# Performance work log

Hardware: AMD Instinct MI355X
Metric: run time of the kernel (lower is better)

## Reference

```python
import jax, jax.numpy as jnp
import numpy as np

N = 100000
E = 1600000
F_IN = 128
HDIM = 64
HEADS = 8
C1 = HDIM // HEADS  # 8 per-head channels in conv1
NUM_CLASSES = 2
NUM_GRAPHS = 64
NEG_SLOPE = 0.2


def setup_inputs() -> dict:
    key = jax.random.key(0)
    ks = jax.random.split(key, 12)
    x = jax.random.normal(ks[0], (N, F_IN), dtype=jnp.float32)
    edge_index = jax.random.randint(ks[1], (2, E), 0, N, dtype=jnp.int64)
    batch = jnp.sort(jax.random.randint(ks[2], (N,), 0, NUM_GRAPHS, dtype=jnp.int64))
    # conv1 params (Glorot-ish scale)
    W1 = jax.random.normal(ks[3], (F_IN, HEADS * C1), dtype=jnp.float32) * (1.0 / np.sqrt(F_IN))
    att_src1 = jax.random.normal(ks[4], (HEADS, C1), dtype=jnp.float32) * 0.1
    att_dst1 = jax.random.normal(ks[5], (HEADS, C1), dtype=jnp.float32) * 0.1
    b1 = jnp.zeros((HEADS * C1,), dtype=jnp.float32)
    # conv2 params (1 head, no concat)
    W2 = jax.random.normal(ks[6], (HDIM, 1 * NUM_CLASSES), dtype=jnp.float32) * (1.0 / np.sqrt(HDIM))
    att_src2 = jax.random.normal(ks[7], (1, NUM_CLASSES), dtype=jnp.float32) * 0.1
    att_dst2 = jax.random.normal(ks[8], (1, NUM_CLASSES), dtype=jnp.float32) * 0.1
    b2 = jnp.zeros((NUM_CLASSES,), dtype=jnp.float32)
    return {"x": x, "edge_index": edge_index, "batch": batch,
            "W1": W1, "att_src1": att_src1, "att_dst1": att_dst1, "b1": b1,
            "W2": W2, "att_src2": att_src2, "att_dst2": att_dst2, "b2": b2}


def gat_conv(x, src, dst, W, a_src, a_dst, b, heads, ch, concat):
    # PyG GATConv: linear proj -> per-edge attention -> segment softmax over dst -> scatter-add
    n = x.shape[0]
    h = (x @ W).reshape(n, heads, ch)                      # [N,H,C]
    alpha_s = jnp.einsum('nhc,hc->nh', h, a_src)           # [N,H]
    alpha_d = jnp.einsum('nhc,hc->nh', h, a_dst)           # [N,H]
    e = jax.nn.leaky_relu(alpha_s[src] + alpha_d[dst], NEG_SLOPE)  # [E,H]
    m = jax.ops.segment_max(e, dst, num_segments=n)        # stable softmax per dst
    e = jnp.exp(e - m[dst])
    denom = jax.ops.segment_sum(e, dst, num_segments=n) + 1e-16
    alpha = e / denom[dst]                                 # [E,H]
    msg = h[src] * alpha[:, :, None]                       # [E,H,C]
    out = jax.ops.segment_sum(msg, dst, num_segments=n)    # [N,H,C]
    if concat:
        out = out.reshape(n, heads * ch)
    else:
        out = out.mean(axis=1)
    return out + b


def reference(x, edge_index, batch, W1, att_src1, att_dst1, b1, W2, att_src2, att_dst2, b2):
    # PyG GATConv default add_self_loops=True
    loops = jnp.arange(N, dtype=edge_index.dtype)
    src = jnp.concatenate([edge_index[0], loops])
    dst = jnp.concatenate([edge_index[1], loops])
    h = gat_conv(x, src, dst, W1, att_src1, att_dst1, b1, HEADS, C1, concat=True)
    h = jax.nn.relu(h)
    # F.dropout with training=False (eval mode) -> identity
    h = gat_conv(h, src, dst, W2, att_src2, att_dst2, b2, 1, NUM_CLASSES, concat=False)
    # global_mean_pool over batch ids
    sums = jax.ops.segment_sum(h, batch, num_segments=NUM_GRAPHS)
    cnts = jax.ops.segment_sum(jnp.ones((N,), h.dtype), batch, num_segments=NUM_GRAPHS)
    pooled = sums / jnp.maximum(cnts, 1.0)[:, None]        # [G, num_classes]
    return jax.nn.log_softmax(pooled, axis=1)
```

## Files before the change

### kernel.cpp

```cpp
#include <hip/hip_runtime.h>
#include <hip/hip_bf16.h>
#include <hip/hip_fp16.h>
#include <math.h>

#define NN 100000
#define EE 1600000
#define ET 1700000
#define NEG_SLOPE 0.2f
#define XS_STRIDE 136

#define BKB 8
#define BKSZ 256
#define NBUCK 391
#define SLAB 8192
#define PAD 32
#define EPT2 16
#define CHUNK2 (256 * EPT2)
#define NCH2 ((ET + CHUNK2 - 1) / CHUNK2)

typedef _Float16 f16;
typedef f16 f16x8 __attribute__((ext_vector_type(8)));
typedef float f32x4 __attribute__((ext_vector_type(4)));

__device__ __forceinline__ float leaky(float v) {
    return v > 0.f ? v : NEG_SLOPE * v;
}
__device__ __forceinline__ unsigned char enc_fp8(float v) {
    int pk = __builtin_amdgcn_cvt_pk_fp8_f32(v, 0.f, 0, false);
    return (unsigned char)(pk & 0xff);
}

__global__ __launch_bounds__(256) void convert_w_kernel(
        const float* __restrict__ W1, f16* __restrict__ wt) {
    int i = blockIdx.x * 256 + threadIdx.x;
    if (i < 128 * 64) {
        int n = i >> 7, k = i & 127;
        wt[n * 128 + k] = (f16)W1[k * 64 + n];
    }
}

__global__ __launch_bounds__(256) void gemm1_mfma(
        const float* __restrict__ x, const f16* __restrict__ wt,
        const float* __restrict__ att_s, const float* __restrict__ att_d,
        unsigned char* __restrict__ h1f8, __half* __restrict__ as1h,
        float* __restrict__ ad1o) {
    __shared__ f16 xs[64 * XS_STRIDE];
    const int tid = threadIdx.x;
    const int node0 = blockIdx.x * 64;
    for (int i = tid; i < 64 * 64; i += 256) {
        int r = i >> 6, cp = i & 63;
        int n = node0 + r;
        float2 v = (n < NN) ? ((const float2*)x)[(long)n * 64 + cp]
                            : make_float2(0.f, 0.f);
        xs[r * XS_STRIDE + 2 * cp]     = (f16)v.x;
        xs[r * XS_STRIDE + 2 * cp + 1] = (f16)v.y;
    }
    __syncthreads();
    const int wv = tid >> 6;
    const int lane = tid & 63;
    const int n16 = lane & 15;
    const int quad = lane >> 4;
    f16x8 bf[4][4];
#pragma unroll
    for (int t = 0; t < 4; ++t)
#pragma unroll
        for (int kk = 0; kk < 4; ++kk)
            bf[t][kk] = *(const f16x8*)(wt + ((t * 16 + n16) * 128 + kk * 32 + quad * 8));
    f32x4 acc[4] = {{0,0,0,0},{0,0,0,0},{0,0,0,0},{0,0,0,0}};
#pragma unroll
    for (int kk = 0; kk < 4; ++kk) {
        f16x8 af = *(const f16x8*)(xs + ((wv * 16 + n16) * XS_STRIDE + kk * 32 + quad * 8));
#pragma unroll
        for (int t = 0; t < 4; ++t)
            acc[t] = __builtin_amdgcn_mfma_f32_16x16x32_f16(af, bf[t][kk], acc[t], 0, 0, 0);
    }
    float ats[4], atd[4];
#pragma unroll
    for (int t = 0; t < 4; ++t) {
        ats[t] = att_s[t * 16 + n16];
        atd[t] = att_d[t * 16 + n16];
    }
#pragma unroll
    for (int t = 0; t < 4; ++t)
#pragma unroll
        for (int r = 0; r < 4; ++r) {
            int m = node0 + wv * 16 + quad * 4 + r;
            bool ok = (m < NN);
            if (ok) h1f8[m * 64 + t * 16 + n16] = enc_fp8(acc[t][r]);
            float vs = acc[t][r] * ats[t];
            float vd = acc[t][r] * atd[t];
            vs += __shfl_xor(vs, 1, 64); vd += __shfl_xor(vd, 1, 64);
            vs += __shfl_xor(vs, 2, 64); vd += __shfl_xor(vd, 2, 64);
            vs += __shfl_xor(vs, 4, 64); vd += __shfl_xor(vd, 4, 64);
            if (ok && (n16 & 7) == 0) {
                int h = t * 2 + (n16 >> 3);
                as1h[m * 8 + h] = __float2half_rn(vs);
                ad1o[m * 8 + h] = vd;
            }
        }
}

__global__ __launch_bounds__(256) void bucket_fill(
        const int* __restrict__ ei, int* __restrict__ bcur,
        unsigned* __restrict__ gpay) {
    __shared__ int lcnt[NBUCK];
    __shared__ int gbase[NBUCK];
    const int tid = threadIdx.x;
    for (int i = tid; i < NBUCK; i += 256) lcnt[i] = 0;
    __syncthreads();
    const int base = blockIdx.x * CHUNK2 + tid;
    unsigned pay[EPT2];
    int bk[EPT2], pos[EPT2];
#pragma unroll
    for (int k = 0; k < EPT2; ++k) {
        int e = base + k * 256;
        if (e < ET) {
            int s, d;
            if (e < EE) {
                s = __builtin_nontemporal_load(ei + e);
                d = __builtin_nontemporal_load(ei + EE + e);
            } else { s = d = e - EE; }
            int b = d >> BKB;
            bk[k] = b;
            pay[k] = ((unsigned)(d & (BKSZ - 1)) << 17) | (unsigned)s;
            pos[k] = atomicAdd(&lcnt[b], 1);
        } else bk[k] = -1;
    }
    __syncthreads();
    for (int i = tid; i < NBUCK; i += 256)
        gbase[i] = lcnt[i] ? (i * SLAB + atomicAdd(&bcur[i * PAD], lcnt[i])) : 0;
    __syncthreads();
#pragma unroll
    for (int k = 0; k < EPT2; ++k)
        if (bk[k] >= 0) gpay[gbase[bk[k]] + pos[k]] = pay[k];
}

__global__ __launch_bounds__(256) void fine_csr(
        const unsigned* __restrict__ gpay, const int* __restrict__ bcur,
        int* __restrict__ rowptr, int* __restrict__ rowend,
        int* __restrict__ csr_src) {
    __shared__ int cnt[BKSZ];
    __shared__ int ts[256];
    const int b = blockIdx.x;
    const int tid = threadIdx.x;
    const int off = b * SLAB;
    int blen = bcur[b * PAD];
    if (blen > SLAB) blen = SLAB;
    const int d0 = b << BKB;
    cnt[tid] = 0;
    __syncthreads();
    for (int i = tid; i < blen; i += 256)
        atomicAdd(&cnt[gpay[off + i] >> 17], 1);
    __syncthreads();
    int v = cnt[tid];
    ts[tid] = v;
    __syncthreads();
    for (int o = 1; o < 256; o <<= 1) {
        int u = (tid >= o) ? ts[tid - o] : 0;
        __syncthreads();
        ts[tid] += u;
        __syncthreads();
    }
    int excl = ts[tid] - v;
    cnt[tid] = excl;
    int d = d0 + tid;
    if (d < NN) {
        rowptr[d] = off + excl;
        rowend[d] = off + excl + v;
    }
    __syncthreads();
    for (int i = tid; i < blen; i += 256) {
        unsigned pay = gpay[off + i];
        int pos = atomicAdd(&cnt[pay >> 17], 1);
        csr_src[off + pos] = (int)(pay & 0x1FFFFu);
    }
}

__global__ __launch_bounds__(256) void conv1_fused_kernel(
        const int* __restrict__ rowptr, const int* __restrict__ rowend,
        const int* __restrict__ csr_src, const __half* __restrict__ as1h,
        const float* __restrict__ ad1,
        const unsigned char* __restrict__ h1f8, const float* __restrict__ b1,
        const float* __restrict__ W2, const float* __restrict__ as2,
        const float* __restrict__ ad2, float4* __restrict__ rec) {
    const int tid = threadIdx.x;
    const int wv = tid >> 6;
    const int c = tid & 63;
    int n0 = __builtin_amdgcn_readfirstlane((blockIdx.x * 4 + wv) * 2);
    int n1 = n0 + 1;
    int h = c >> 3;
    int kB = c >> 3;
    int hB = c & 7;
    float adA = ad1[n0 * 8 + hB], adB = ad1[n1 * 8 + hB];
    float adhA = ad1[n0 * 8 + h],  adhB = ad1[n1 * 8 + h];
    const int bperm_base = h << 2;
    int jA = rowptr[n0], eA = rowend[n0];
    int jB = rowptr[n1], eB = rowend[n1];
    float lA0 = 0.f, lA1 = 0.f, aA0 = 0.f, aA1 = 0.f;
    float lB0 = 0.f, lB1 = 0.f, aB0 = 0.f, aB1 = 0.f;
    while (jA + 7 < eA && jB + 7 < eB) {
        int mySA = csr_src[jA + kB];
        int mySB = csr_src[jB + kB];
        float pA = __expf(leaky(__half2float(as1h[mySA * 8 + hB]) + adA));
        float pB = __expf(leaky(__half2float(as1h[mySB * 8 + hB]) + adB));
        int piA = __float_as_int(pA), piB = __float_as_int(pB);
#pragma unroll
        for (int k = 0; k < 8; ++k) {
            int skA = csr_src[jA + k];
            int skB = csr_src[jB + k];
            float pkA = __int_as_float(
                __builtin_amdgcn_ds_bpermute(bperm_base + (k << 5), piA));
            float pkB = __int_as_float(
                __builtin_amdgcn_ds_bpermute(bperm_base + (k << 5), piB));
            float fkA = __builtin_amdgcn_cvt_f32_fp8((int)h1f8[skA * 64 + c], 0);
            float fkB = __builtin_amdgcn_cvt_f32_fp8((int)h1f8[skB * 64 + c], 0);
            if (k & 1) { lA1 += pkA; aA1 += pkA * fkA; lB1 += pkB; aB1 += pkB * fkB; }
            else       { lA0 += pkA; aA0 += pkA * fkA; lB0 += pkB; aB0 += pkB * fkB; }
        }
        jA += 8; jB += 8;
    }
    for (; jA + 7 < eA; jA += 8) {
        int myS = csr_src[jA + kB];
        float myp = __expf(leaky(__half2float(as1h[myS * 8 + hB]) + adA));
        int mypi = __float_as_int(myp);
#pragma unroll
        for (int k = 0; k < 8; ++k) {
            int sk = csr_src[jA + k];
            float pk = __int_as_float(
                __builtin_amdgcn_ds_bpermute(bperm_base + (k << 5), mypi));
            float fk = __builtin_amdgcn_cvt_f32_fp8((int)h1f8[sk * 64 + c], 0);
            if (k & 1) { lA1 += pk; aA1 += pk * fk; }
            else       { lA0 += pk; aA0 += pk * fk; }
        }
    }
    for (; jA < eA; ++jA) {
        int s = csr_src[jA];
        float p = __expf(leaky(__half2float(as1h[s * 8 + h]) + adhA));
        float f = __builtin_amdgcn_cvt_f32_fp8((int)h1f8[s * 64 + c], 0);
        lA0 += p; aA0 += p * f;
    }
    for (; jB + 7 < eB; jB += 8) {
        int myS = csr_src[jB + kB];
        float myp = __expf(leaky(__half2float(as1h[myS * 8 + hB]) + adB));
        int mypi = __float_as_int(myp);
#pragma unroll
        for (int k = 0; k < 8; ++k) {
            int sk = csr_src[jB + k];
            float pk = __int_as_float(
                __builtin_amdgcn_ds_bpermute(bperm_base + (k << 5), mypi));
            float fk = __builtin_amdgcn_cvt_f32_fp8((int)h1f8[sk * 64 + c], 0);
            if (k & 1) { lB1 += pk; aB1 += pk * fk; }
            else       { lB0 += pk; aB0 += pk * fk; }
        }
    }
    for (; jB < eB; ++jB) {
        int s = csr_src[jB];
        float p = __expf(leaky(__half2float(as1h[s * 8 + h]) + adhB));
        float f = __builtin_amdgcn_cvt_f32_fp8((int)h1f8[s * 64 + c], 0);
        lB0 += p; aB0 += p * f;
    }
    float lA = lA0 + lA1, accA = aA0 + aA1;
    float lB = lB0 + lB1, accB = aB0 + aB1;
    float aAv = accA / (lA + 1e-16f) + b1[c];
    float aBv = accB / (lB + 1e-16f) + b1[c];
    aAv = aAv > 0.f ? aAv : 0.f;
    aBv = aBv > 0.f ? aBv : 0.f;
    float w20 = W2[c * 2], w21 = W2[c * 2 + 1];
    float rA0 = aAv * w20, rA1 = aAv * w21;
    float rB0 = aBv * w20, rB1 = aBv * w21;
#pragma unroll
    for (int off = 32; off > 0; off >>= 1) {
        rA0 += __shfl_xor(rA0, off, 64);
        rA1 += __shfl_xor(rA1, off, 64);
        rB0 += __shfl_xor(rB0, off, 64);
        rB1 += __shfl_xor(rB1, off, 64);
    }
    if (c == 0) {
        rec[n0] = make_float4(rA0 * as2[0] + rA1 * as2[1], rA0, rA1,
                              rA0 * ad2[0] + rA1 * ad2[1]);
        rec[n1] = make_float4(rB0 * as2[0] + rB1 * as2[1], rB0, rB1,
                              rB0 * ad2[0] + rB1 * ad2[1]);
    }
}

__global__ __launch_bounds__(256) void conv2_pool_kernel(
        const int* __restrict__ rowptr, const int* __restrict__ rowend,
        const int* __restrict__ csr_src, const float4* __restrict__ rec,
        const int* __restrict__ batch,
        float* __restrict__ pooled ) {
    __shared__ float ls[192];
    int tid = threadIdx.x;
    if (tid < 192) ls[tid] = 0.f;
    __syncthreads();
    int n = blockIdx.x * 256 + tid;
    if (n < NN) {
        float adn = rec[n].w;
        int jb = rowptr[n], je = rowend[n];
        float l0 = 0.f, l1 = 0.f, l2 = 0.f, l3 = 0.f;
        float x0 = 0.f, x1 = 0.f, x2 = 0.f, x3 = 0.f;
        float y0 = 0.f, y1 = 0.f, y2 = 0.f, y3 = 0.f;
        int j = jb;
        for (; j + 3 < je; j += 4) {
            float4 ra = rec[csr_src[j]];
            float4 rb = rec[csr_src[j + 1]];
            float4 rc = rec[csr_src[j + 2]];
            float4 rd = rec[csr_src[j + 3]];
            float pa = __expf(leaky(ra.x + adn));
            float pb = __expf(leaky(rb.x + adn));
            float pc = __expf(leaky(rc.x + adn));
            float pd = __expf(leaky(rd.x + adn));
            l0 += pa; x0 += pa * ra.y; y0 += pa * ra.z;
            l1 += pb; x1 += pb * rb.y; y1 += pb * rb.z;
            l2 += pc; x2 += pc * rc.y; y2 += pc * rc.z;
            l3 += pd; x3 += pd * rd.y; y3 += pd * rd.z;
        }
        for (; j < je; ++j) {
            float4 ra = rec[csr_src[j]];
            float pa = __expf(leaky(ra.x + adn));
            l0 += pa; x0 += pa * ra.y; y0 += pa * ra.z;
        }
        float l = (l0 + l1) + (l2 + l3);
        float xx = (x0 + x1) + (x2 + x3);
        float yy = (y0 + y1) + (y2 + y3);
        float inv = 1.f / (l + 1e-16f);
        int g = batch[n];
        atomicAdd(&ls[g * 2],     xx * inv);
        atomicAdd(&ls[g * 2 + 1], yy * inv);
        atomicAdd(&ls[128 + g],   1.f);
    }
    __syncthreads();
    if (tid < 192) atomicAdd(&pooled[tid], ls[tid]);
}

__global__ __launch_bounds__(64) void final_kernel(
        const float* __restrict__ pooled, const float* __restrict__ b2,
        float* __restrict__ out) {
    int g = threadIdx.x;
    if (g >= 64) return;
    float c = pooled[128 + g];
    float denom = c > 1.f ? c : 1.f;
    float p0 = pooled[g * 2] / denom + b2[0];
    float p1 = pooled[g * 2 + 1] / denom + b2[1];
    float m = fmaxf(p0, p1);
    float lse = m + logf(expf(p0 - m) + expf(p1 - m));
    out[g * 2] = p0 - lse;
    out[g * 2 + 1] = p1 - lse;
}

extern "C" void kernel_launch(void* const* d_in, const int* in_sizes, int n_in,
                              void* d_out, int out_size, void* d_ws, size_t ws_size,
                              hipStream_t stream) {
    const float* x   = (const float*)d_in[0];
    const int*   ei  = (const int*)d_in[1];
    const int*   bat = (const int*)d_in[2];
    const float* W1  = (const float*)d_in[3];
    const float* as1 = (const float*)d_in[4];
    const float* ad1 = (const float*)d_in[5];
    const float* b1  = (const float*)d_in[6];
    const float* W2  = (const float*)d_in[7];
    const float* as2 = (const float*)d_in[8];
    const float* ad2 = (const float*)d_in[9];
    const float* b2  = (const float*)d_in[10];
    float* out = (float*)d_out;

    float* ws = (float*)d_ws;
    const long off_h1f8   = 0;
    const long off_wt     = off_h1f8 + (long)NN * 16;
    const long off_as1h   = off_wt   + 4096;
    const long off_ad1    = off_as1h + (long)NN * 4;
    const long off_rec    = off_ad1  + (long)NN * 8;
    const long off_rowptr = off_rec  + (long)NN * 4;
    const long off_rowend = off_rowptr + NN;
    const long off_gpay   = off_rowend + NN;
    const long off_csr    = off_gpay + (long)NBUCK * SLAB;
    const long off_zero   = off_csr  + (long)NBUCK * SLAB;
    const long off_bcur   = off_zero;
    const long off_pool   = off_bcur + NBUCK * PAD;
    const long zero_elems = off_pool + 192 - off_zero;

    hipMemsetAsync(ws + off_zero, 0, zero_elems * sizeof(float), stream);

    convert_w_kernel<<<32, 256, 0, stream>>>(W1, (f16*)(ws + off_wt));
    gemm1_mfma<<<(NN + 63) / 64, 256, 0, stream>>>(
        x, (const f16*)(ws + off_wt), as1, ad1,
        (unsigned char*)(ws + off_h1f8), (__half*)(ws + off_as1h),
        ws + off_ad1);

    bucket_fill<<<NCH2, 256, 0, stream>>>(ei, (int*)(ws + off_bcur),
                                          (unsigned*)(ws + off_gpay));
    fine_csr<<<NBUCK, 256, 0, stream>>>(
        (const unsigned*)(ws + off_gpay), (const int*)(ws + off_bcur),
        (int*)(ws + off_rowptr), (int*)(ws + off_rowend),
        (int*)(ws + off_csr));

    conv1_fused_kernel<<<NN / 8, 256, 0, stream>>>(
        (const int*)(ws + off_rowptr), (const int*)(ws + off_rowend),
        (const int*)(ws + off_csr), (const __half*)(ws + off_as1h),
        ws + off_ad1, (const unsigned char*)(ws + off_h1f8),
        b1, W2, as2, ad2, (float4*)(ws + off_rec));

    conv2_pool_kernel<<<(NN + 255) / 256, 256, 0, stream>>>(
        (const int*)(ws + off_rowptr), (const int*)(ws + off_rowend),
        (const int*)(ws + off_csr), (const float4*)(ws + off_rec),
        bat, ws + off_pool);

    final_kernel<<<1, 64, 0, stream>>>(ws + off_pool, b2, out);
}
```

Measured before the change: 253.2 us.

## Restructure conv1 aggregation so each lane handles one edge-head with 8-byte fp8 loads

New measurement: 236.7 us. 1.07x faster.

```diff
diff --git a/kernel.cpp b/kernel.cpp
--- a/kernel.cpp
+++ b/kernel.cpp
@@ -21,6 +21,7 @@
 typedef _Float16 f16;
 typedef f16 f16x8 __attribute__((ext_vector_type(8)));
 typedef float f32x4 __attribute__((ext_vector_type(4)));
+typedef float f32x2 __attribute__((ext_vector_type(2)));
 
 __device__ __forceinline__ float leaky(float v) {
     return v > 0.f ? v : NEG_SLOPE * v;
@@ -186,90 +187,78 @@
     const int tid = threadIdx.x;
     const int wv = tid >> 6;
     const int c = tid & 63;
+    const int slot = c >> 3;
+    const int hd = c & 7;
     int n0 = __builtin_amdgcn_readfirstlane((blockIdx.x * 4 + wv) * 2);
     int n1 = n0 + 1;
-    int h = c >> 3;
-    int kB = c >> 3;
-    int hB = c & 7;
-    float adA = ad1[n0 * 8 + hB], adB = ad1[n1 * 8 + hB];
-    float adhA = ad1[n0 * 8 + h],  adhB = ad1[n1 * 8 + h];
-    const int bperm_base = h << 2;
+    const float adA = ad1[n0 * 8 + hd];
+    const float adB = ad1[n1 * 8 + hd];
     int jA = rowptr[n0], eA = rowend[n0];
     int jB = rowptr[n1], eB = rowend[n1];
-    float lA0 = 0.f, lA1 = 0.f, aA0 = 0.f, aA1 = 0.f;
-    float lB0 = 0.f, lB1 = 0.f, aB0 = 0.f, aB1 = 0.f;
-    while (jA + 7 < eA && jB + 7 < eB) {
-        int mySA = csr_src[jA + kB];
-        int mySB = csr_src[jB + kB];
-        float pA = __expf(leaky(__half2float(as1h[mySA * 8 + hB]) + adA));
-        float pB = __expf(leaky(__half2float(as1h[mySB * 8 + hB]) + adB));
-        int piA = __float_as_int(pA), piB = __float_as_int(pB);
-#pragma unroll
-        for (int k = 0; k < 8; ++k) {
-            int skA = csr_src[jA + k];
-            int skB = csr_src[jB + k];
-            float pkA = __int_as_float(
-                __builtin_amdgcn_ds_bpermute(bperm_base + (k << 5), piA));
-            float pkB = __int_as_float(
-                __builtin_amdgcn_ds_bpermute(bperm_base + (k << 5), piB));
-            float fkA = __builtin_amdgcn_cvt_f32_fp8((int)h1f8[skA * 64 + c], 0);
-            float fkB = __builtin_amdgcn_cvt_f32_fp8((int)h1f8[skB * 64 + c], 0);
-            if (k & 1) { lA1 += pkA; aA1 += pkA * fkA; lB1 += pkB; aB1 += pkB * fkB; }
-            else       { lA0 += pkA; aA0 += pkA * fkA; lB0 += pkB; aB0 += pkB * fkB; }
+    float accA[8] = {0.f,0.f,0.f,0.f,0.f,0.f,0.f,0.f};
+    float accB[8] = {0.f,0.f,0.f,0.f,0.f,0.f,0.f,0.f};
+    float lA = 0.f, lB = 0.f;
+
+#define STEP1(j, e, ad, l, acc)                                              \
+    {                                                                        \
+        int rem = (e) - (j);                                                 \
+        int sl = slot < rem ? slot : rem - 1;                                \
+        int src = csr_src[(j) + sl];                                         \
+        float p = __expf(leaky(__half2float(as1h[src * 8 + hd]) + (ad)));    \
+        if (slot >= rem) p = 0.f;                                            \
+        uint2 fb = *(const uint2*)(h1f8 + src * 64 + hd * 8);                \
+        f32x2 f01 = __builtin_amdgcn_cvt_pk_f32_fp8((int)fb.x, 0);           \
+        f32x2 f23 = __builtin_amdgcn_cvt_pk_f32_fp8((int)fb.x, 1);           \
+        f32x2 f45 = __builtin_amdgcn_cvt_pk_f32_fp8((int)fb.y, 0);           \
+        f32x2 f67 = __builtin_amdgcn_cvt_pk_f32_fp8((int)fb.y, 1);           \
+        (l) += p;                                                            \
+        acc[0] += p * f01.x; acc[1] += p * f01.y;                            \
+        acc[2] += p * f23.x; acc[3] += p * f23.y;                            \
+        acc[4] += p * f45.x; acc[5] += p * f45.y;                            \
+        acc[6] += p * f67.x; acc[7] += p * f67.y;                            \
+        (j) += 8;                                                            \
+    }
+
+    while (jA < eA && jB < eB) {
+        STEP1(jA, eA, adA, lA, accA);
+        STEP1(jB, eB, adB, lB, accB);
+    }
+    while (jA < eA) STEP1(jA, eA, adA, lA, accA);
+    while (jB < eB) STEP1(jB, eB, adB, lB, accB);
+#undef STEP1
+
+#pragma unroll
+    for (int off = 8; off <= 32; off <<= 1) {
+        lA += __shfl_xor(lA, off, 64);
+        lB += __shfl_xor(lB, off, 64);
+#pragma unroll
+        for (int i = 0; i < 8; ++i) {
+            accA[i] += __shfl_xor(accA[i], off, 64);
+            accB[i] += __shfl_xor(accB[i], off, 64);
         }
-        jA += 8; jB += 8;
-    }
-    for (; jA + 7 < eA; jA += 8) {
-        int myS = csr_src[jA + kB];
-        float myp = __expf(leaky(__half2float(as1h[myS * 8 + hB]) + adA));
-        int mypi = __float_as_int(myp);
-#pragma unroll
-        for (int k = 0; k < 8; ++k) {
-            int sk = csr_src[jA + k];
-            float pk = __int_as_float(
-                __builtin_amdgcn_ds_bpermute(bperm_base + (k << 5), mypi));
-            float fk = __builtin_amdgcn_cvt_f32_fp8((int)h1f8[sk * 64 + c], 0);
-            if (k & 1) { lA1 += pk; aA1 += pk * fk; }
-            else       { lA0 += pk; aA0 += pk * fk; }
-        }
-    }
-    for (; jA < eA; ++jA) {
-        int s = csr_src[jA];
-        float p = __expf(leaky(__half2float(as1h[s * 8 + h]) + adhA));
-        float f = __builtin_amdgcn_cvt_f32_fp8((int)h1f8[s * 64 + c], 0);
-        lA0 += p; aA0 += p * f;
-    }
-    for (; jB + 7 < eB; jB += 8) {
-        int myS = csr_src[jB + kB];
-        float myp = __expf(leaky(__half2float(as1h[myS * 8 + hB]) + adB));
-        int mypi = __float_as_int(myp);
-#pragma unroll
-        for (int k = 0; k < 8; ++k) {
-            int sk = csr_src[jB + k];
-            float pk = __int_as_float(
-                __builtin_amdgcn_ds_bpermute(bperm_base + (k << 5), mypi));
-            float fk = __builtin_amdgcn_cvt_f32_fp8((int)h1f8[sk * 64 + c], 0);
-            if (k & 1) { lB1 += pk; aB1 += pk * fk; }
-            else       { lB0 += pk; aB0 += pk * fk; }
-        }
-    }
-    for (; jB < eB; ++jB) {
-        int s = csr_src[jB];
-        float p = __expf(leaky(__half2float(as1h[s * 8 + h]) + adhB));
-        float f = __builtin_amdgcn_cvt_f32_fp8((int)h1f8[s * 64 + c], 0);
-        lB0 += p; aB0 += p * f;
-    }
-    float lA = lA0 + lA1, accA = aA0 + aA1;
-    float lB = lB0 + lB1, accB = aB0 + aB1;
-    float aAv = accA / (lA + 1e-16f) + b1[c];
-    float aBv = accB / (lB + 1e-16f) + b1[c];
-    aAv = aAv > 0.f ? aAv : 0.f;
-    aBv = aBv > 0.f ? aBv : 0.f;
-    float w20 = W2[c * 2], w21 = W2[c * 2 + 1];
-    float rA0 = aAv * w20, rA1 = aAv * w21;
-    float rB0 = aBv * w20, rB1 = aBv * w21;
-#pragma unroll
-    for (int off = 32; off > 0; off >>= 1) {
+    }
+    const float invA = 1.f / (lA + 1e-16f);
+    const float invB = 1.f / (lB + 1e-16f);
+    const float4* b1v = (const float4*)(b1 + hd * 8);
+    const float4* w2v = (const float4*)(W2 + hd * 16);
+    float bb[8], ww[16];
+    *(float4*)(bb)     = b1v[0]; *(float4*)(bb + 4)  = b1v[1];
+    *(float4*)(ww)     = w2v[0]; *(float4*)(ww + 4)  = w2v[1];
+    *(float4*)(ww + 8) = w2v[2]; *(float4*)(ww + 12) = w2v[3];
+    float rA0 = 0.f, rA1 = 0.f, rB0 = 0.f, rB1 = 0.f;
+#pragma unroll
+    for (int i = 0; i < 8; ++i) {
+        float aAv = accA[i] * invA + bb[i];
+        float aBv = accB[i] * invB + bb[i];
+        aAv = aAv > 0.f ? aAv : 0.f;
+        aBv = aBv > 0.f ? aBv : 0.f;
+        rA0 += aAv * ww[2 * i];
+        rA1 += aAv * ww[2 * i + 1];
+        rB0 += aBv * ww[2 * i];
+        rB1 += aBv * ww[2 * i + 1];
+    }
+#pragma unroll
+    for (int off = 1; off <= 4; off <<= 1) {
         rA0 += __shfl_xor(rA0, off, 64);
         rA1 += __shfl_xor(rA1, off, 64);
         rB0 += __shfl_xor(rB0, off, 64);
```
